# Kernel tuning notes

Measured on AMD Instinct MI355X. Metric: run time of the kernel, lower is better.

The kernel has to match this reference:

```python
import jax, jax.numpy as jnp
import numpy as np

B, S, V, E, H, M, OOV = 64, 400, 50000, 128, 512, 512, 20


def setup_inputs() -> dict:
    key = jax.random.key(0)
    ks = jax.random.split(key, 24)
    d = {}
    d["y"] = jax.random.randint(ks[0], (B,), 0, V)
    d["h"] = jax.random.normal(ks[1], (1, B, H), jnp.float32)
    d["memory_bank"] = jax.random.normal(ks[2], (B, S, M), jnp.float32)
    d["src_mask"] = jnp.ones((B, S), jnp.float32)
    d["max_num_oovs"] = OOV
    d["src_oov"] = jax.random.randint(ks[3], (B, S), 0, V + OOV)
    d["coverage"] = jax.random.uniform(ks[4], (B, S), jnp.float32)
    # parameters (torch Linear convention: W [out, in])
    sc = 0.02
    d["emb_W"] = jax.random.normal(ks[5], (V, E), jnp.float32) * sc
    d["gru_W_ih"] = jax.random.normal(ks[6], (3 * H, E), jnp.float32) * sc
    d["gru_W_hh"] = jax.random.normal(ks[7], (3 * H, H), jnp.float32) * sc
    d["gru_b_ih"] = jnp.zeros((3 * H,), jnp.float32)
    d["gru_b_hh"] = jnp.zeros((3 * H,), jnp.float32)
    d["attn_Wm"] = jax.random.normal(ks[8], (H, M), jnp.float32) * sc
    d["attn_Wd"] = jax.random.normal(ks[9], (H, H), jnp.float32) * sc
    d["attn_bd"] = jnp.zeros((H,), jnp.float32)
    d["attn_Wc"] = jax.random.normal(ks[10], (H, 1), jnp.float32) * sc
    d["attn_v"] = jax.random.normal(ks[11], (H,), jnp.float32) * sc
    d["pgen_W"] = jax.random.normal(ks[12], (1, E + H + M), jnp.float32) * sc
    d["pgen_b"] = jnp.zeros((1,), jnp.float32)
    d["vd1_W"] = jax.random.normal(ks[13], (H, H + M), jnp.float32) * sc
    d["vd1_b"] = jnp.zeros((H,), jnp.float32)
    d["vd2_W"] = jax.random.normal(ks[14], (V, H), jnp.float32) * sc
    d["vd2_b"] = jnp.zeros((V,), jnp.float32)
    return d


def _decode_step(y, h, memory_bank, src_mask, max_num_oovs, src_oov, coverage,
                 emb_W, gru_W_ih, gru_W_hh, gru_b_ih, gru_b_hh,
                 attn_Wm, attn_Wd, attn_bd, attn_Wc, attn_v,
                 pgen_W, pgen_b, vd1_W, vd1_b, vd2_W, vd2_b):
    bsz = src_oov.shape[0]
    y_emb = emb_W[y]                                   # [B,E]
    # --- single-step GRU (num_layers=1, torch gate layout r,z,n) ---
    h0 = h[0]                                          # [B,H]
    gi = y_emb @ gru_W_ih.T + gru_b_ih                 # [B,3H]
    gh = h0 @ gru_W_hh.T + gru_b_hh                    # [B,3H]
    i_r, i_z, i_n = jnp.split(gi, 3, axis=-1)
    h_r, h_z, h_n = jnp.split(gh, 3, axis=-1)
    r = jax.nn.sigmoid(i_r + h_r)
    z = jax.nn.sigmoid(i_z + h_z)
    n = jnp.tanh(i_n + r * h_n)
    h1 = (1.0 - z) * n + z * h0                        # [B,H]
    h_next = h1[None]                                  # [1,B,H]
    # --- additive (concat) attention with coverage ---
    enc_feat = memory_bank @ attn_Wm.T                 # [B,S,H]
    dec_feat = h1 @ attn_Wd.T + attn_bd                # [B,H]
    cov_feat = coverage[..., None] * attn_Wc[:, 0]     # [B,S,H]
    scores = jnp.tanh(enc_feat + dec_feat[:, None, :] + cov_feat) @ attn_v  # [B,S]
    scores = jnp.where(src_mask > 0, scores, -1e9)
    attn = jax.nn.softmax(scores, axis=1) * src_mask
    attn = attn / (attn.sum(axis=1, keepdims=True) + 1e-10)  # masked softmax
    word_context = jnp.einsum('bs,bsm->bm', attn, memory_bank)
    coverage_next = coverage + attn
    # --- vocab distribution ---
    vocab_in = jnp.concatenate([word_context, h1], axis=1)   # [B,M+H]
    hid = vocab_in @ vd1_W.T + vd1_b
    vocab_dist = jax.nn.softmax(hid @ vd2_W.T + vd2_b, axis=1)  # [B,V]
    # --- pointer-generator merge ---
    pgen_in = jnp.concatenate([word_context, h1, y_emb], axis=1)
    p_gen = jax.nn.sigmoid(pgen_in @ pgen_W.T + pgen_b)      # [B,1]
    vocab_dist_ = p_gen * vocab_dist
    attn_dist_ = (1.0 - p_gen) * attn
    if max_num_oovs > 0:
        vocab_dist_ = jnp.concatenate(
            [vocab_dist_, jnp.zeros((bsz, max_num_oovs), vocab_dist_.dtype)], axis=1)
    rows = jnp.arange(bsz)[:, None]
    final_dist = vocab_dist_.at[rows, src_oov].add(attn_dist_)  # [B,V+OOV]
    return final_dist, h_next, word_context, attn, p_gen, coverage_next


def reference(y, h, memory_bank, src_mask, max_num_oovs, src_oov, coverage,
              emb_W, gru_W_ih, gru_W_hh, gru_b_ih, gru_b_hh,
              attn_Wm, attn_Wd, attn_bd, attn_Wc, attn_v,
              pgen_W, pgen_b, vd1_W, vd1_b, vd2_W, vd2_b):
    return _decode_step(y, h, memory_bank, src_mask, max_num_oovs, src_oov, coverage,
                        emb_W, gru_W_ih, gru_W_hh, gru_b_ih, gru_b_hh,
                        attn_Wm, attn_Wd, attn_bd, attn_Wc, attn_v,
                        pgen_W, pgen_b, vd1_W, vd1_b, vd2_W, vd2_b)
```

## Files before the change

kernel.cpp:

```cpp
#include <hip/hip_runtime.h>

typedef unsigned short u16;
typedef unsigned int u32;
using bf16x8 = __attribute__((ext_vector_type(8))) short;
using f32x4  = __attribute__((ext_vector_type(4))) float;

#define B_ 64
#define S_ 400
#define E_ 128
#define H_ 512
#define M_ 512
#define R_ (B_ * S_)

__device__ __forceinline__ float b2f(u16 u){
  union { u32 i; float f; } c; c.i = ((u32)u) << 16; return c.f;
}
__device__ __forceinline__ u16 f2b(float f){
  union { u32 i; float f; } c; c.f = f;
  u32 r = c.i + 0x7FFFu + ((c.i >> 16) & 1u);
  return (u16)(r >> 16);
}
__device__ __forceinline__ float sigm(float x){ return 1.0f / (1.0f + __expf(-x)); }
__device__ __forceinline__ float fast_tanh(float x){
  float e = __expf(2.0f * x);
  return 1.0f - 2.0f / (e + 1.0f);
}
__device__ __forceinline__ bf16x8 pack8(const float* __restrict__ p){
  const u32* u = (const u32*)p;
  union { u32 w[4]; bf16x8 v; } c;
  c.w[0] = (u[1] & 0xFFFF0000u) | (u[0] >> 16);
  c.w[1] = (u[3] & 0xFFFF0000u) | (u[2] >> 16);
  c.w[2] = (u[5] & 0xFFFF0000u) | (u[4] >> 16);
  c.w[3] = (u[7] & 0xFFFF0000u) | (u[6] >> 16);
  return c.v;
}
__device__ __forceinline__ bf16x8 pack8r(float4 a, float4 b){
  union { u32 w[4]; bf16x8 v; } c;
  c.w[0] = (__float_as_uint(a.y) & 0xFFFF0000u) | (__float_as_uint(a.x) >> 16);
  c.w[1] = (__float_as_uint(a.w) & 0xFFFF0000u) | (__float_as_uint(a.z) >> 16);
  c.w[2] = (__float_as_uint(b.y) & 0xFFFF0000u) | (__float_as_uint(b.x) >> 16);
  c.w[3] = (__float_as_uint(b.w) & 0xFFFF0000u) | (__float_as_uint(b.z) >> 16);
  return c.v;
}

__global__ void k0_zero(float* __restrict__ scores, float* __restrict__ ctx_ws,
                        float* __restrict__ yemb_ws,
                        const int* __restrict__ y, const float* __restrict__ embW,
                        const float* __restrict__ Wm, u16* __restrict__ wmbf){
  int i = blockIdx.x * 256 + threadIdx.x;
  if (i < R_) { scores[i] = 0.f; return; }
  i -= R_;
  if (i < B_ * M_) { ctx_ws[i] = 0.f; return; }
  i -= B_ * M_;
  if (i < B_ * E_) {
    int b = i >> 7, e = i & 127;
    yemb_ws[i] = embW[(size_t)y[b] * E_ + e];
    return;
  }
  i -= B_ * E_;
  if (i < (H_ * M_) / 8) {
    int j16 = i >> 10;
    int rem = i & 1023;
    int ks  = rem >> 6;
    int l   = rem & 63;
    int row = j16 * 16 + (l & 15);
    int col = ks * 32 + (l >> 4) * 8;
    *(bf16x8*)(wmbf + (size_t)i * 8) = pack8(Wm + (size_t)row * 512 + col);
  }
}

__global__ __launch_bounds__(256) void k1a_gru(
    const float* __restrict__ h, const float* __restrict__ yemb_ws,
    const float* __restrict__ Wih, const float* __restrict__ Whh,
    const float* __restrict__ bih, const float* __restrict__ bhh,
    float* __restrict__ h1_ws, float* __restrict__ h_out)
{
  __shared__ float red_r[4][64], red_z[4][64], red_nh[4][64], red_ni[4][64];
  int hh = blockIdx.x;
  int t = threadIdx.x, w = t >> 6, lane = t & 63;
  const float* xrow = h + lane * H_;
  const float* erow = yemb_ws + lane * E_;
  const float* wr = Whh + (size_t)hh * H_;
  const float* wz = Whh + (size_t)(hh + H_) * H_;
  const float* wn = Whh + (size_t)(hh + 2 * H_) * H_;
  float pr = 0.f, pz = 0.f, pnh = 0.f, pni = 0.f;
  int k0 = w * 128;
  #pragma unroll 8
  for (int k = k0; k < k0 + 128; k += 4){
    float4 x = *(const float4*)(xrow + k);
    float4 a = *(const float4*)(wr + k);
    float4 bq = *(const float4*)(wz + k);
    float4 c = *(const float4*)(wn + k);
    pr  += a.x*x.x + a.y*x.y + a.z*x.z + a.w*x.w;
    pz  += bq.x*x.x + bq.y*x.y + bq.z*x.z + bq.w*x.w;
    pnh += c.x*x.x + c.y*x.y + c.z*x.z + c.w*x.w;
  }
  const float* ur = Wih + (size_t)hh * E_;
  const float* uz = Wih + (size_t)(hh + H_) * E_;
  const float* un = Wih + (size_t)(hh + 2 * H_) * E_;
  int e0 = w * 32;
  #pragma unroll
  for (int k = e0; k < e0 + 32; k += 4){
    float4 x = *(const float4*)(erow + k);
    float4 a = *(const float4*)(ur + k);
    float4 bq = *(const float4*)(uz + k);
    float4 c = *(const float4*)(un + k);
    pr  += a.x*x.x + a.y*x.y + a.z*x.z + a.w*x.w;
    pz  += bq.x*x.x + bq.y*x.y + bq.z*x.z + bq.w*x.w;
    pni += c.x*x.x + c.y*x.y + c.z*x.z + c.w*x.w;
  }
  red_r[w][lane] = pr; red_z[w][lane] = pz;
  red_nh[w][lane] = pnh; red_ni[w][lane] = pni;
  __syncthreads();
  if (t < 64){
    int b = t;
    float rr = bih[hh] + bhh[hh];
    float zz = bih[H_ + hh] + bhh[H_ + hh];
    float nh = bhh[2 * H_ + hh];
    float ni = bih[2 * H_ + hh];
    #pragma unroll
    for (int ww = 0; ww < 4; ww++){
      rr += red_r[ww][b]; zz += red_z[ww][b];
      nh += red_nh[ww][b]; ni += red_ni[ww][b];
    }
    float r = sigm(rr), z = sigm(zz);
    float n = fast_tanh(ni + r * nh);
    float h0v = h[b * H_ + hh];
    float h1v = (1.0f - z) * n + z * h0v;
    h1_ws[b * H_ + hh] = h1v;
    h_out[b * H_ + hh] = h1v;
  }
}

__global__ __launch_bounds__(256) void k1b_dec(
    const float* __restrict__ h1_ws, const float* __restrict__ Wd,
    const float* __restrict__ bd, float* __restrict__ dec_ws)
{
  __shared__ float red[4][64];
  int hh = blockIdx.x;
  int t = threadIdx.x, w = t >> 6, lane = t & 63;
  const float* xrow = h1_ws + lane * H_;
  const float* wd = Wd + (size_t)hh * H_;
  float p = 0.f;
  int k0 = w * 128;
  #pragma unroll 8
  for (int k = k0; k < k0 + 128; k += 4){
    float4 x = *(const float4*)(xrow + k);
    float4 a = *(const float4*)(wd + k);
    p += a.x*x.x + a.y*x.y + a.z*x.z + a.w*x.w;
  }
  red[w][lane] = p;
  __syncthreads();
  if (t < 64){
    float s = bd[hh] + red[0][t] + red[1][t] + red[2][t] + red[3][t];
    dec_ws[t * H_ + hh] = s;
  }
}

__global__ __launch_bounds__(512) void k2_scores(
    const float* __restrict__ mb, const u16* __restrict__ wmbf,
    const float* __restrict__ dec, const float* __restrict__ cov,
    const float* __restrict__ Wc, const float* __restrict__ av,
    float* __restrict__ scores)
{
  __shared__ u16 alds[2][32 * 128];
  int t = threadIdx.x;
  int lane = t & 63, w = t >> 6;
  int quad = lane >> 4, l16 = lane & 15;
  int rowB = blockIdx.x * 32;
  int cb = w * 64;
  f32x4 acc[2][4];
  #pragma unroll
  for (int rg = 0; rg < 2; rg++)
    #pragma unroll
    for (int j = 0; j < 4; j++) acc[rg][j] = (f32x4){0.f,0.f,0.f,0.f};

  int srow = t >> 4, sg8 = t & 15;
  int sw0 = srow * 128 + 8 * (sg8 ^ (srow & 7));
  {
    const float* g0 = mb + (size_t)(rowB + srow) * 512 + sg8 * 8;
    float4 a0 = *(const float4*)g0, b0 = *(const float4*)(g0 + 4);
    *(bf16x8*)&alds[0][sw0] = pack8r(a0, b0);
  }
  const u16* wlane = wmbf + lane * 8;
  bf16x8 bcur[4];
  #pragma unroll
  for (int j = 0; j < 4; j++)
    bcur[j] = *(const bf16x8*)(wlane + (size_t)((w * 4 + j) * 16) * 512);
  __syncthreads();
  for (int c = 0; c < 4; c++){
    float4 pa0, pb0;
    if (c < 3){
      const float* g0 = mb + (size_t)(rowB + srow) * 512 + (c + 1) * 128 + sg8 * 8;
      pa0 = *(const float4*)g0; pb0 = *(const float4*)(g0 + 4);
    }
    const u16* buf = alds[c & 1];
    #pragma unroll
    for (int s = 0; s < 4; s++){
      bf16x8 bnxt[4];
      bool more = (s < 3) || (c < 3);
      if (more){
        int kn = c * 4 + s + 1;
        #pragma unroll
        for (int j = 0; j < 4; j++)
          bnxt[j] = *(const bf16x8*)(wlane + (size_t)((w * 4 + j) * 16 + kn) * 512);
      }
      bf16x8 af[2];
      #pragma unroll
      for (int rg = 0; rg < 2; rg++)
        af[rg] = *(const bf16x8*)&buf[(rg * 16 + l16) * 128 + 8 * ((s * 4 + quad) ^ (l16 & 7))];
      #pragma unroll
      for (int j = 0; j < 4; j++)
        #pragma unroll
        for (int rg = 0; rg < 2; rg++)
          acc[rg][j] = __builtin_amdgcn_mfma_f32_16x16x32_bf16(af[rg], bcur[j], acc[rg][j], 0, 0, 0);
      if (more){
        #pragma unroll
        for (int j = 0; j < 4; j++) bcur[j] = bnxt[j];
      }
    }
    if (c < 3){
      u16* d = (u16*)alds[(c + 1) & 1];
      *(bf16x8*)&d[sw0] = pack8r(pa0, pb0);
    }
    __syncthreads();
  }
  float vv[4], wcv[4];
  #pragma unroll
  for (int j = 0; j < 4; j++){
    int hc = cb + j * 16 + l16;
    vv[j] = av[hc]; wcv[j] = Wc[hc];
  }
  #pragma unroll
  for (int rg = 0; rg < 2; rg++){
    #pragma unroll
    for (int r = 0; r < 4; r++){
      int R = rowB + rg * 16 + quad * 4 + r;
      int bb = R / S_;
      float cf = cov[R];
      const float* decb = dec + bb * H_;
      float sum = 0.f;
      #pragma unroll
      for (int j = 0; j < 4; j++){
        int hc = cb + j * 16 + l16;
        float e = acc[rg][j][r] + decb[hc] + cf * wcv[j];
        sum += fast_tanh(e) * vv[j];
      }
      #pragma unroll
      for (int m = 1; m < 16; m <<= 1) sum += __shfl_xor(sum, m, 64);
      if (l16 == 0) atomicAdd(&scores[R], sum);
    }
  }
}

__global__ __launch_bounds__(256) void k3a_softmax(
    const float* __restrict__ scores, const float* __restrict__ mask,
    const float* __restrict__ cov,
    float* __restrict__ attn_ws,
    float* __restrict__ out_attn, float* __restrict__ out_cov)
{
  __shared__ float p_s[S_];
  __shared__ float m_s[S_];
  __shared__ float red[256];
  int b = blockIdx.x, t = threadIdx.x;
  float lmax = -3.0e38f;
  for (int s = t; s < S_; s += 256){
    float mk = mask[b*S_ + s];
    float v = scores[b*S_ + s];
    v = (mk > 0.f) ? v : -1e9f;
    p_s[s] = v; m_s[s] = mk;
    lmax = fmaxf(lmax, v);
  }
  red[t] = lmax; __syncthreads();
  for (int o = 128; o > 0; o >>= 1){ if (t < o) red[t] = fmaxf(red[t], red[t+o]); __syncthreads(); }
  float MX = red[0]; __syncthreads();
  float lsum = 0.f;
  for (int s = t; s < S_; s += 256){ float e = __expf(p_s[s] - MX); p_s[s] = e; lsum += e; }
  red[t] = lsum; __syncthreads();
  for (int o = 128; o > 0; o >>= 1){ if (t < o) red[t] += red[t+o]; __syncthreads(); }
  float inv1 = 1.0f / red[0]; __syncthreads();
  float l2 = 0.f;
  for (int s = t; s < S_; s += 256){ float a = p_s[s] * inv1 * m_s[s]; p_s[s] = a; l2 += a; }
  red[t] = l2; __syncthreads();
  for (int o = 128; o > 0; o >>= 1){ if (t < o) red[t] += red[t+o]; __syncthreads(); }
  float inv2 = 1.0f / (red[0] + 1e-10f); __syncthreads();
  for (int s = t; s < S_; s += 256){
    float a = p_s[s] * inv2;
    attn_ws[b*S_ + s] = a;
    out_attn[b*S_ + s] = a;
    out_cov[b*S_ + s]  = cov[b*S_ + s] + a;
  }
}

__global__ __launch_bounds__(256) void k3b_ctx(
    const float* __restrict__ attn_ws, const float* __restrict__ mb,
    float* __restrict__ ctx_ws)
{
  int b = blockIdx.x, sc = blockIdx.y, t = threadIdx.x;
  int m0 = t * 2;
  const float* mbb = mb + (size_t)b * S_ * M_;
  const float* ab  = attn_ws + b * S_;
  float a0 = 0.f, a1 = 0.f;
  int s0 = sc * 25;
  for (int s = s0; s < s0 + 25; s++){
    float a = ab[s];
    float2 c = *(const float2*)(mbb + s*M_ + m0);
    a0 += a * c.x;
    a1 += a * c.y;
  }
  atomicAdd(&ctx_ws[b*M_ + m0],     a0);
  atomicAdd(&ctx_ws[b*M_ + m0 + 1], a1);
}

__global__ __launch_bounds__(256) void k4a_hid(
    const float* __restrict__ ctx_ws, const float* __restrict__ h1_ws,
    const float* __restrict__ vd1W, const float* __restrict__ vd1b,
    u16* __restrict__ hid_bf)
{
  __shared__ float red[4][64];
  int hh = blockIdx.x;
  int t = threadIdx.x, w = t >> 6, lane = t & 63;
  int k0 = w * 256;
  const float* xbase = (w < 2) ? (ctx_ws + lane * 512 + k0)
                               : (h1_ws + lane * 512 + (k0 - 512));
  const float* wrow = vd1W + (size_t)hh * 1024 + k0;
  float p = 0.f;
  #pragma unroll 8
  for (int k = 0; k < 256; k += 4){
    float4 x = *(const float4*)(xbase + k);
    float4 a = *(const float4*)(wrow + k);
    p += a.x*x.x + a.y*x.y + a.z*x.z + a.w*x.w;
  }
  red[w][lane] = p;
  __syncthreads();
  if (t < 64){
    float s = vd1b[hh] + red[0][t] + red[1][t] + red[2][t] + red[3][t];
    hid_bf[t * 512 + hh] = f2b(s);
  }
}

__global__ __launch_bounds__(128) void k4b_pgen(
    const float* __restrict__ ctx_ws, const float* __restrict__ h1_ws,
    const float* __restrict__ yemb_ws,
    const float* __restrict__ pgW, const float* __restrict__ pgb,
    float* __restrict__ pgen_ws, float* __restrict__ out_pgen,
    float* __restrict__ out_ctx)
{
  __shared__ float red[128];
  int b = blockIdx.x, t = threadIdx.x;
  float p = 0.f;
  for (int i = t; i < 1152; i += 128){
    float x = (i < 512) ? ctx_ws[b * 512 + i]
            : (i < 1024) ? h1_ws[b * 512 + (i - 512)]
                         : yemb_ws[b * 128 + (i - 1024)];
    p += x * pgW[i];
  }
  red[t] = p; __syncthreads();
  for (int o = 64; o > 0; o >>= 1){ if (t < o) red[t] += red[t + o]; __syncthreads(); }
  if (t == 0){
    float pg = sigm(red[0] + pgb[0]);
    pgen_ws[b] = pg; out_pgen[b] = pg;
  }
  for (int i = t; i < 512; i += 128)
    out_ctx[b * 512 + i] = ctx_ws[b * 512 + i];
}

__global__ __launch_bounds__(256) void k5_logits(
    const u16* __restrict__ hid_bf, const float* __restrict__ vd2W,
    const float* __restrict__ vd2b, int V, u16* __restrict__ logits_bf)
{
  __shared__ u16 blds[2][64 * 128];
  int t = threadIdx.x;
  int lane = t & 63, w = t >> 6;
  int quad = lane >> 4, l16 = lane & 15;
  int cb = blockIdx.x * 64;
  f32x4 acc[4];
  #pragma unroll
  for (int rg = 0; rg < 4; rg++) acc[rg] = (f32x4){0.f,0.f,0.f,0.f};

  int scol0 = t >> 4, sg8 = t & 15;
  {
    #pragma unroll
    for (int i = 0; i < 4; i++){
      int col = scol0 + i * 16;
      int gr = cb + col; if (gr > V - 1) gr = V - 1;
      const float* gs = vd2W + (size_t)gr * 512 + sg8 * 8;
      float4 x = *(const float4*)gs, yv = *(const float4*)(gs + 4);
      *(bf16x8*)&blds[0][col * 128 + 8 * (sg8 ^ (col & 7))] = pack8r(x, yv);
    }
  }
  __syncthreads();
  int cw = w * 16 + l16;
  for (int c = 0; c < 4; c++){
    float4 px0, py0, px1, py1, px2, py2, px3, py3;
    if (c < 3){
      int kc = (c + 1) * 128;
      int g0 = cb + scol0;      if (g0 > V-1) g0 = V-1;
      int g1 = cb + scol0 + 16; if (g1 > V-1) g1 = V-1;
      int g2 = cb + scol0 + 32; if (g2 > V-1) g2 = V-1;
      int g3 = cb + scol0 + 48; if (g3 > V-1) g3 = V-1;
      const float* s0 = vd2W + (size_t)g0 * 512 + kc + sg8 * 8;
      const float* s1 = vd2W + (size_t)g1 * 512 + kc + sg8 * 8;
      const float* s2 = vd2W + (size_t)g2 * 512 + kc + sg8 * 8;
      const float* s3 = vd2W + (size_t)g3 * 512 + kc + sg8 * 8;
      px0 = *(const float4*)s0; py0 = *(const float4*)(s0 + 4);
      px1 = *(const float4*)s1; py1 = *(const float4*)(s1 + 4);
      px2 = *(const float4*)s2; py2 = *(const float4*)(s2 + 4);
      px3 = *(const float4*)s3; py3 = *(const float4*)(s3 + 4);
    }
    bf16x8 aF[4][4];
    #pragma unroll
    for (int s = 0; s < 4; s++)
      #pragma unroll
      for (int rg = 0; rg < 4; rg++)
        aF[s][rg] = *(const bf16x8*)(hid_bf + (size_t)(rg * 16 + l16) * 512 + c * 128 + s * 32 + quad * 8);
    const u16* buf = blds[c & 1];
    #pragma unroll
    for (int s = 0; s < 4; s++){
      bf16x8 bfb = *(const bf16x8*)&buf[cw * 128 + 8 * ((s * 4 + quad) ^ (cw & 7))];
      #pragma unroll
      for (int rg = 0; rg < 4; rg++)
        acc[rg] = __builtin_amdgcn_mfma_f32_16x16x32_bf16(aF[s][rg], bfb, acc[rg], 0, 0, 0);
    }
    if (c < 3){
      u16* d = (u16*)blds[(c + 1) & 1];
      *(bf16x8*)&d[scol0 * 128        + 8 * (sg8 ^ (scol0 & 7))]        = pack8r(px0, py0);
      *(bf16x8*)&d[(scol0+16) * 128   + 8 * (sg8 ^ ((scol0+16) & 7))]   = pack8r(px1, py1);
      *(bf16x8*)&d[(scol0+32) * 128   + 8 * (sg8 ^ ((scol0+32) & 7))]   = pack8r(px2, py2);
      *(bf16x8*)&d[(scol0+48) * 128   + 8 * (sg8 ^ ((scol0+48) & 7))]   = pack8r(px3, py3);
    }
    __syncthreads();
  }
  int v = cb + w * 16 + l16;
  if (v < V){
    float bias = vd2b[v];
    #pragma unroll
    for (int rg = 0; rg < 4; rg++){
      #pragma unroll
      for (int r = 0; r < 4; r++){
        int bb = rg * 16 + quad * 4 + r;
        logits_bf[(size_t)bb * V + v] = f2b(acc[rg][r] + bias);
      }
    }
  }
}

__global__ __launch_bounds__(256) void k6a_partial(
    const u16* __restrict__ logits_bf, int V,
    float* __restrict__ mxp, float* __restrict__ denp)
{
  __shared__ float red[256];
  int b = blockIdx.x, ch = blockIdx.y, t = threadIdx.x;
  int VG = V >> 3;
  int per = (VG + 7) >> 3;
  int g0 = ch * per;
  int g1 = g0 + per; if (g1 > VG) g1 = VG;
  const bf16x8* row = (const bf16x8*)(logits_bf + (size_t)b * V);
  float x[32];
  float m = -3.0e38f;
  #pragma unroll
  for (int i = 0; i < 4; i++){
    int g = g0 + t + i * 256;
    bool ok = g < g1;
    bf16x8 v;
    if (ok) v = row[g];
    #pragma unroll
    for (int j = 0; j < 8; j++){
      float f = ok ? b2f((u16)v[j]) : -3.0e38f;
      x[i * 8 + j] = f;
      m = fmaxf(m, f);
    }
  }
  red[t] = m; __syncthreads();
  for (int o = 128; o > 0; o >>= 1){ if (t < o) red[t] = fmaxf(red[t], red[t+o]); __syncthreads(); }
  float MX = red[0]; __syncthreads();
  float s = 0.f;
  #pragma unroll
  for (int k = 0; k < 32; k++) s += __expf(x[k] - MX);
  red[t] = s; __syncthreads();
  for (int o = 128; o > 0; o >>= 1){ if (t < o) red[t] += red[t+o]; __syncthreads(); }
  if (t == 0){ mxp[b * 8 + ch] = MX; denp[b * 8 + ch] = red[0]; }
}

__global__ void k6b_combine(const float* __restrict__ mxp, const float* __restrict__ denp,
                            float* __restrict__ mx_ws, float* __restrict__ den_ws)
{
  int b = threadIdx.x;
  float M = -3.0e38f;
  #pragma unroll
  for (int c = 0; c < 8; c++) M = fmaxf(M, mxp[b * 8 + c]);
  float d = 0.f;
  #pragma unroll
  for (int c = 0; c < 8; c++) d += denp[b * 8 + c] * __expf(mxp[b * 8 + c] - M);
  mx_ws[b] = M; den_ws[b] = d;
}

__global__ void k7a_vocab(const u16* __restrict__ logits_bf,
    const float* __restrict__ mx_ws, const float* __restrict__ den_ws,
    const float* __restrict__ pgen_ws, int V, int VO, float* __restrict__ out_final)
{
  int b = blockIdx.y;
  int c = (blockIdx.x * 256 + threadIdx.x) * 4;
  if (c >= VO) return;
  float MX = mx_ws[b];
  float inv = pgen_ws[b] / den_ws[b];
  float v4[4] = {0.f, 0.f, 0.f, 0.f};
  if (c + 3 < V){
    ushort4 u = *(const ushort4*)(logits_bf + (size_t)b * V + c);
    v4[0] = inv * __expf(b2f(u.x) - MX);
    v4[1] = inv * __expf(b2f(u.y) - MX);
    v4[2] = inv * __expf(b2f(u.z) - MX);
    v4[3] = inv * __expf(b2f(u.w) - MX);
  } else {
    #pragma unroll
    for (int j = 0; j < 4; j++){
      int cc = c + j;
      if (cc < V) v4[j] = inv * __expf(b2f(logits_bf[(size_t)b * V + cc]) - MX);
    }
  }
  if (c + 4 <= VO){
    *(float4*)(out_final + (size_t)b * VO + c) = make_float4(v4[0], v4[1], v4[2], v4[3]);
  } else {
    for (int j = 0; j < 4 && c + j < VO; j++) out_final[(size_t)b * VO + c + j] = v4[j];
  }
}

__global__ void k7b_scatter(const int* __restrict__ src_oov,
    const float* __restrict__ attn_ws, const float* __restrict__ pgen_ws,
    int VO, float* __restrict__ out_final)
{
  int idx = blockIdx.x * 256 + threadIdx.x;
  if (idx >= R_) return;
  int b = idx / S_;
  float ad = (1.0f - pgen_ws[b]) * attn_ws[idx];
  atomicAdd(&out_final[(size_t)b*VO + src_oov[idx]], ad);
}

extern "C" void kernel_launch(void* const* d_in, const int* in_sizes, int n_in,
                              void* d_out, int out_size, void* d_ws, size_t ws_size,
                              hipStream_t stream)
{
  const int*   y      = (const int*)d_in[0];
  const float* h      = (const float*)d_in[1];
  const float* mb     = (const float*)d_in[2];
  const float* mask   = (const float*)d_in[3];
  const int*   srcoov = (const int*)d_in[5];
  const float* cov    = (const float*)d_in[6];
  const float* embW   = (const float*)d_in[7];
  const float* Wih    = (const float*)d_in[8];
  const float* Whh    = (const float*)d_in[9];
  const float* bih    = (const float*)d_in[10];
  const float* bhh    = (const float*)d_in[11];
  const float* Wm     = (const float*)d_in[12];
  const float* Wd     = (const float*)d_in[13];
  const float* bd     = (const float*)d_in[14];
  const float* Wc     = (const float*)d_in[15];
  const float* av     = (const float*)d_in[16];
  const float* pgW    = (const float*)d_in[17];
  const float* pgb    = (const float*)d_in[18];
  const float* vd1W   = (const float*)d_in[19];
  const float* vd1b   = (const float*)d_in[20];
  const float* vd2W   = (const float*)d_in[21];
  const float* vd2b   = (const float*)d_in[22];

  const int V  = in_sizes[22];
  const int VO = (int)((long long)out_size / B_ - (H_ + M_ + 2*S_ + 1));

  float* out = (float*)d_out;
  float* out_final = out;
  float* out_h     = out_final + (size_t)B_ * VO;
  float* out_ctx   = out_h     + (size_t)B_ * H_;
  float* out_attn  = out_ctx   + (size_t)B_ * M_;
  float* out_pgen  = out_attn  + (size_t)B_ * S_;
  float* out_cov   = out_pgen  + B_;

  float* ws      = (float*)d_ws;
  float* scores  = ws;
  float* h1_ws   = ws + 25600;
  float* yemb_ws = ws + 58368;
  float* dec_ws  = ws + 66560;
  float* attn_ws = ws + 99328;
  float* ctx_ws  = ws + 124928;
  float* pgen_ws = ws + 157696;
  float* mx_ws   = ws + 157760;
  float* den_ws  = ws + 157824;
  u16*   hid_bf    = (u16*)(ws + 157888);
  u16*   logits_bf = (u16*)(ws + 174272);
  u16*   wm_bf     = logits_bf;
  float* mxp_ws  = scores;
  float* denp_ws = scores + 512;

  hipLaunchKernelGGL(k0_zero,    dim3(388),  dim3(256), 0, stream,
                     scores, ctx_ws, yemb_ws, y, embW, Wm, wm_bf);
  hipLaunchKernelGGL(k1a_gru,    dim3(512),  dim3(256), 0, stream,
                     h, yemb_ws, Wih, Whh, bih, bhh, h1_ws, out_h);
  hipLaunchKernelGGL(k1b_dec,    dim3(512),  dim3(256), 0, stream,
                     h1_ws, Wd, bd, dec_ws);
  hipLaunchKernelGGL(k2_scores,  dim3(800),  dim3(512), 0, stream,
                     mb, wm_bf, dec_ws, cov, Wc, av, scores);
  hipLaunchKernelGGL(k3a_softmax, dim3(64),  dim3(256), 0, stream,
                     scores, mask, cov, attn_ws, out_attn, out_cov);
  hipLaunchKernelGGL(k3b_ctx,    dim3(64, 16), dim3(256), 0, stream,
                     attn_ws, mb, ctx_ws);
  hipLaunchKernelGGL(k4a_hid,    dim3(512),  dim3(256), 0, stream,
                     ctx_ws, h1_ws, vd1W, vd1b, hid_bf);
  hipLaunchKernelGGL(k4b_pgen,   dim3(64),   dim3(128), 0, stream,
                     ctx_ws, h1_ws, yemb_ws, pgW, pgb, pgen_ws, out_pgen, out_ctx);
  hipLaunchKernelGGL(k5_logits,  dim3((V + 63) / 64), dim3(256), 0, stream,
                     hid_bf, vd2W, vd2b, V, logits_bf);
  hipLaunchKernelGGL(k6a_partial, dim3(64, 8), dim3(256), 0, stream,
                     logits_bf, V, mxp_ws, denp_ws);
  hipLaunchKernelGGL(k6b_combine, dim3(1),   dim3(64), 0, stream,
                     mxp_ws, denp_ws, mx_ws, den_ws);
  hipLaunchKernelGGL(k7a_vocab,  dim3((VO + 1023) / 1024, 64), dim3(256), 0, stream,
                     logits_bf, mx_ws, den_ws, pgen_ws, V, VO, out_final);
  hipLaunchKernelGGL(k7b_scatter, dim3(100), dim3(256), 0, stream,
                     srcoov, attn_ws, pgen_ws, VO, out_final);
}
```

Measured before the change: 390.7 us.

## Fuse softmax combine into vocab kernel, LDS-reduce scores, widen GEMV blocks

Drops the k6b_combine launch: every k7a_vocab block now recombines the 8 per-chunk max/denominator partials itself. Attention scores are accumulated with LDS atomics and written once per block, so the global zeroing of scores in k0 goes away. The GRU, decoder-projection and hidden GEMV kernels move to 512-thread blocks that split K across 8 waves, and the out_ctx copy moves from k4b_pgen into k4a_hid. The cost is some redundant per-block recombine work and larger reduction trees.

```diff
diff --git a/kernel.cpp b/kernel.cpp
--- a/kernel.cpp
+++ b/kernel.cpp
@@ -43,13 +43,11 @@
   return c.v;
 }
 
-__global__ void k0_zero(float* __restrict__ scores, float* __restrict__ ctx_ws,
+__global__ void k0_zero(float* __restrict__ ctx_ws,
                         float* __restrict__ yemb_ws,
                         const int* __restrict__ y, const float* __restrict__ embW,
                         const float* __restrict__ Wm, u16* __restrict__ wmbf){
   int i = blockIdx.x * 256 + threadIdx.x;
-  if (i < R_) { scores[i] = 0.f; return; }
-  i -= R_;
   if (i < B_ * M_) { ctx_ws[i] = 0.f; return; }
   i -= B_ * M_;
   if (i < B_ * E_) {
@@ -69,13 +67,13 @@
   }
 }
 
-__global__ __launch_bounds__(256) void k1a_gru(
+__global__ __launch_bounds__(512) void k1a_gru(
     const float* __restrict__ h, const float* __restrict__ yemb_ws,
     const float* __restrict__ Wih, const float* __restrict__ Whh,
     const float* __restrict__ bih, const float* __restrict__ bhh,
     float* __restrict__ h1_ws, float* __restrict__ h_out)
 {
-  __shared__ float red_r[4][64], red_z[4][64], red_nh[4][64], red_ni[4][64];
+  __shared__ float red_r[8][64], red_z[8][64], red_nh[8][64], red_ni[8][64];
   int hh = blockIdx.x;
   int t = threadIdx.x, w = t >> 6, lane = t & 63;
   const float* xrow = h + lane * H_;
@@ -84,9 +82,9 @@
   const float* wz = Whh + (size_t)(hh + H_) * H_;
   const float* wn = Whh + (size_t)(hh + 2 * H_) * H_;
   float pr = 0.f, pz = 0.f, pnh = 0.f, pni = 0.f;
-  int k0 = w * 128;
-  #pragma unroll 8
-  for (int k = k0; k < k0 + 128; k += 4){
+  int k0 = w * 64;
+  #pragma unroll
+  for (int k = k0; k < k0 + 64; k += 4){
     float4 x = *(const float4*)(xrow + k);
     float4 a = *(const float4*)(wr + k);
     float4 bq = *(const float4*)(wz + k);
@@ -98,9 +96,9 @@
   const float* ur = Wih + (size_t)hh * E_;
   const float* uz = Wih + (size_t)(hh + H_) * E_;
   const float* un = Wih + (size_t)(hh + 2 * H_) * E_;
-  int e0 = w * 32;
-  #pragma unroll
-  for (int k = e0; k < e0 + 32; k += 4){
+  int e0 = w * 16;
+  #pragma unroll
+  for (int k = e0; k < e0 + 16; k += 4){
     float4 x = *(const float4*)(erow + k);
     float4 a = *(const float4*)(ur + k);
     float4 bq = *(const float4*)(uz + k);
@@ -119,7 +117,7 @@
     float nh = bhh[2 * H_ + hh];
     float ni = bih[2 * H_ + hh];
     #pragma unroll
-    for (int ww = 0; ww < 4; ww++){
+    for (int ww = 0; ww < 8; ww++){
       rr += red_r[ww][b]; zz += red_z[ww][b];
       nh += red_nh[ww][b]; ni += red_ni[ww][b];
     }
@@ -132,19 +130,19 @@
   }
 }
 
-__global__ __launch_bounds__(256) void k1b_dec(
+__global__ __launch_bounds__(512) void k1b_dec(
     const float* __restrict__ h1_ws, const float* __restrict__ Wd,
     const float* __restrict__ bd, float* __restrict__ dec_ws)
 {
-  __shared__ float red[4][64];
+  __shared__ float red[8][64];
   int hh = blockIdx.x;
   int t = threadIdx.x, w = t >> 6, lane = t & 63;
   const float* xrow = h1_ws + lane * H_;
   const float* wd = Wd + (size_t)hh * H_;
   float p = 0.f;
-  int k0 = w * 128;
-  #pragma unroll 8
-  for (int k = k0; k < k0 + 128; k += 4){
+  int k0 = w * 64;
+  #pragma unroll
+  for (int k = k0; k < k0 + 64; k += 4){
     float4 x = *(const float4*)(xrow + k);
     float4 a = *(const float4*)(wd + k);
     p += a.x*x.x + a.y*x.y + a.z*x.z + a.w*x.w;
@@ -152,7 +150,9 @@
   red[w][lane] = p;
   __syncthreads();
   if (t < 64){
-    float s = bd[hh] + red[0][t] + red[1][t] + red[2][t] + red[3][t];
+    float s = bd[hh];
+    #pragma unroll
+    for (int ww = 0; ww < 8; ww++) s += red[ww][t];
     dec_ws[t * H_ + hh] = s;
   }
 }
@@ -164,6 +164,7 @@
     float* __restrict__ scores)
 {
   __shared__ u16 alds[2][32 * 128];
+  __shared__ float sc_lds[32];
   int t = threadIdx.x;
   int lane = t & 63, w = t >> 6;
   int quad = lane >> 4, l16 = lane & 15;
@@ -174,6 +175,8 @@
   for (int rg = 0; rg < 2; rg++)
     #pragma unroll
     for (int j = 0; j < 4; j++) acc[rg][j] = (f32x4){0.f,0.f,0.f,0.f};
+
+  if (t < 32) sc_lds[t] = 0.f;
 
   int srow = t >> 4, sg8 = t & 15;
   int sw0 = srow * 128 + 8 * (sg8 ^ (srow & 7));
@@ -248,9 +251,11 @@
       }
       #pragma unroll
       for (int m = 1; m < 16; m <<= 1) sum += __shfl_xor(sum, m, 64);
-      if (l16 == 0) atomicAdd(&scores[R], sum);
-    }
-  }
+      if (l16 == 0) atomicAdd(&sc_lds[R - rowB], sum);
+    }
+  }
+  __syncthreads();
+  if (t < 32) scores[rowB + t] = sc_lds[t];
 }
 
 __global__ __launch_bounds__(256) void k3a_softmax(
@@ -312,21 +317,21 @@
   atomicAdd(&ctx_ws[b*M_ + m0 + 1], a1);
 }
 
-__global__ __launch_bounds__(256) void k4a_hid(
+__global__ __launch_bounds__(512) void k4a_hid(
     const float* __restrict__ ctx_ws, const float* __restrict__ h1_ws,
     const float* __restrict__ vd1W, const float* __restrict__ vd1b,
-    u16* __restrict__ hid_bf)
-{
-  __shared__ float red[4][64];
+    u16* __restrict__ hid_bf, float* __restrict__ out_ctx)
+{
+  __shared__ float red[8][64];
   int hh = blockIdx.x;
   int t = threadIdx.x, w = t >> 6, lane = t & 63;
-  int k0 = w * 256;
-  const float* xbase = (w < 2) ? (ctx_ws + lane * 512 + k0)
+  int k0 = w * 128;
+  const float* xbase = (w < 4) ? (ctx_ws + lane * 512 + k0)
                                : (h1_ws + lane * 512 + (k0 - 512));
   const float* wrow = vd1W + (size_t)hh * 1024 + k0;
   float p = 0.f;
   #pragma unroll 8
-  for (int k = 0; k < 256; k += 4){
+  for (int k = 0; k < 128; k += 4){
     float4 x = *(const float4*)(xbase + k);
     float4 a = *(const float4*)(wrow + k);
     p += a.x*x.x + a.y*x.y + a.z*x.z + a.w*x.w;
@@ -334,8 +339,11 @@
   red[w][lane] = p;
   __syncthreads();
   if (t < 64){
-    float s = vd1b[hh] + red[0][t] + red[1][t] + red[2][t] + red[3][t];
+    float s = vd1b[hh];
+    #pragma unroll
+    for (int ww = 0; ww < 8; ww++) s += red[ww][t];
     hid_bf[t * 512 + hh] = f2b(s);
+    out_ctx[t * 512 + hh] = ctx_ws[t * 512 + hh];
   }
 }
 
@@ -343,8 +351,7 @@
     const float* __restrict__ ctx_ws, const float* __restrict__ h1_ws,
     const float* __restrict__ yemb_ws,
     const float* __restrict__ pgW, const float* __restrict__ pgb,
-    float* __restrict__ pgen_ws, float* __restrict__ out_pgen,
-    float* __restrict__ out_ctx)
+    float* __restrict__ pgen_ws, float* __restrict__ out_pgen)
 {
   __shared__ float red[128];
   int b = blockIdx.x, t = threadIdx.x;
@@ -361,8 +368,6 @@
     float pg = sigm(red[0] + pgb[0]);
     pgen_ws[b] = pg; out_pgen[b] = pg;
   }
-  for (int i = t; i < 512; i += 128)
-    out_ctx[b * 512 + i] = ctx_ws[b * 512 + i];
 }
 
 __global__ __launch_bounds__(256) void k5_logits(
@@ -482,28 +487,20 @@
   if (t == 0){ mxp[b * 8 + ch] = MX; denp[b * 8 + ch] = red[0]; }
 }
 
-__global__ void k6b_combine(const float* __restrict__ mxp, const float* __restrict__ denp,
-                            float* __restrict__ mx_ws, float* __restrict__ den_ws)
-{
-  int b = threadIdx.x;
-  float M = -3.0e38f;
-  #pragma unroll
-  for (int c = 0; c < 8; c++) M = fmaxf(M, mxp[b * 8 + c]);
-  float d = 0.f;
-  #pragma unroll
-  for (int c = 0; c < 8; c++) d += denp[b * 8 + c] * __expf(mxp[b * 8 + c] - M);
-  mx_ws[b] = M; den_ws[b] = d;
-}
-
 __global__ void k7a_vocab(const u16* __restrict__ logits_bf,
-    const float* __restrict__ mx_ws, const float* __restrict__ den_ws,
+    const float* __restrict__ mxp, const float* __restrict__ denp,
     const float* __restrict__ pgen_ws, int V, int VO, float* __restrict__ out_final)
 {
   int b = blockIdx.y;
+  float MX = -3.0e38f;
+  #pragma unroll
+  for (int cix = 0; cix < 8; cix++) MX = fmaxf(MX, mxp[b * 8 + cix]);
+  float den = 0.f;
+  #pragma unroll
+  for (int cix = 0; cix < 8; cix++) den += denp[b * 8 + cix] * __expf(mxp[b * 8 + cix] - MX);
   int c = (blockIdx.x * 256 + threadIdx.x) * 4;
   if (c >= VO) return;
-  float MX = mx_ws[b];
-  float inv = pgen_ws[b] / den_ws[b];
+  float inv = pgen_ws[b] / den;
   float v4[4] = {0.f, 0.f, 0.f, 0.f};
   if (c + 3 < V){
     ushort4 u = *(const ushort4*)(logits_bf + (size_t)b * V + c);
@@ -582,19 +579,17 @@
   float* attn_ws = ws + 99328;
   float* ctx_ws  = ws + 124928;
   float* pgen_ws = ws + 157696;
-  float* mx_ws   = ws + 157760;
-  float* den_ws  = ws + 157824;
   u16*   hid_bf    = (u16*)(ws + 157888);
   u16*   logits_bf = (u16*)(ws + 174272);
   u16*   wm_bf     = logits_bf;
   float* mxp_ws  = scores;
   float* denp_ws = scores + 512;
 
-  hipLaunchKernelGGL(k0_zero,    dim3(388),  dim3(256), 0, stream,
-                     scores, ctx_ws, yemb_ws, y, embW, Wm, wm_bf);
-  hipLaunchKernelGGL(k1a_gru,    dim3(512),  dim3(256), 0, stream,
+  hipLaunchKernelGGL(k0_zero,    dim3(288),  dim3(256), 0, stream,
+                     ctx_ws, yemb_ws, y, embW, Wm, wm_bf);
+  hipLaunchKernelGGL(k1a_gru,    dim3(512),  dim3(512), 0, stream,
                      h, yemb_ws, Wih, Whh, bih, bhh, h1_ws, out_h);
-  hipLaunchKernelGGL(k1b_dec,    dim3(512),  dim3(256), 0, stream,
+  hipLaunchKernelGGL(k1b_dec,    dim3(512),  dim3(512), 0, stream,
                      h1_ws, Wd, bd, dec_ws);
   hipLaunchKernelGGL(k2_scores,  dim3(800),  dim3(512), 0, stream,
                      mb, wm_bf, dec_ws, cov, Wc, av, scores);
@@ -602,18 +597,16 @@
                      scores, mask, cov, attn_ws, out_attn, out_cov);
   hipLaunchKernelGGL(k3b_ctx,    dim3(64, 16), dim3(256), 0, stream,
                      attn_ws, mb, ctx_ws);
-  hipLaunchKernelGGL(k4a_hid,    dim3(512),  dim3(256), 0, stream,
-                     ctx_ws, h1_ws, vd1W, vd1b, hid_bf);
+  hipLaunchKernelGGL(k4a_hid,    dim3(512),  dim3(512), 0, stream,
+                     ctx_ws, h1_ws, vd1W, vd1b, hid_bf, out_ctx);
   hipLaunchKernelGGL(k4b_pgen,   dim3(64),   dim3(128), 0, stream,
-                     ctx_ws, h1_ws, yemb_ws, pgW, pgb, pgen_ws, out_pgen, out_ctx);
+                     ctx_ws, h1_ws, yemb_ws, pgW, pgb, pgen_ws, out_pgen);
   hipLaunchKernelGGL(k5_logits,  dim3((V + 63) / 64), dim3(256), 0, stream,
                      hid_bf, vd2W, vd2b, V, logits_bf);
   hipLaunchKernelGGL(k6a_partial, dim3(64, 8), dim3(256), 0, stream,
                      logits_bf, V, mxp_ws, denp_ws);
-  hipLaunchKernelGGL(k6b_combine, dim3(1),   dim3(64), 0, stream,
-                     mxp_ws, denp_ws, mx_ws, den_ws);
   hipLaunchKernelGGL(k7a_vocab,  dim3((VO + 1023) / 1024, 64), dim3(256), 0, stream,
-                     logits_bf, mx_ws, den_ws, pgen_ws, V, VO, out_final);
+                     logits_bf, mxp_ws, denp_ws, pgen_ws, V, VO, out_final);
   hipLaunchKernelGGL(k7b_scatter, dim3(100), dim3(256), 0, stream,
                      srcoov, attn_ws, pgen_ws, VO, out_final);
 }
```

New measurement: 386.2 us. Within noise of the previous version (-1.2%).
